# Kernel optimization log

Measured on AMD Instinct MI355X. Metric: run time of the kernel, lower is better.

The kernel has to match this reference:

```python
import jax, jax.numpy as jnp
import numpy as np

D_IN = 768
D_OUT = 768
NUM_HEADS = 12


def setup_inputs() -> dict:
    key = jax.random.key(0)
    kx, kq, kk, kv, ko = jax.random.split(key, 5)
    x = jax.random.normal(kx, (4, 2048, D_IN), dtype=jnp.float32)
    # torch.rand -> uniform [0,1)
    w_query = jax.random.uniform(kq, (D_IN, D_OUT), dtype=jnp.float32)
    w_key = jax.random.uniform(kk, (D_IN, D_OUT), dtype=jnp.float32)
    w_value = jax.random.uniform(kv, (D_IN, D_OUT), dtype=jnp.float32)
    out_proj = jax.random.uniform(ko, (D_IN, D_OUT), dtype=jnp.float32)
    return {"x": x, "w_query": w_query, "w_key": w_key, "w_value": w_value, "out_proj": out_proj}


def reference(x, w_query, w_key, w_value, out_proj):
    b, n, _ = x.shape
    hd = D_OUT // NUM_HEADS  # head_dim
    q = (x @ w_query).reshape(b, n, NUM_HEADS, hd).transpose(0, 2, 1, 3)  # [b,h,n,hd]
    k = (x @ w_key).reshape(b, n, NUM_HEADS, hd).transpose(0, 2, 1, 3)
    v = (x @ w_value).reshape(b, n, NUM_HEADS, hd).transpose(0, 2, 1, 3)
    scores = jnp.einsum('bhqd,bhkd->bhqk', q, k)
    causal = jnp.triu(jnp.ones((n, n), dtype=bool), k=1)
    scores = jnp.where(causal, -jnp.inf, scores)
    attn = jax.nn.softmax(scores / jnp.sqrt(jnp.float32(hd)), axis=-1)
    # dropout p=0.0 -> identity
    ctx = jnp.einsum('bhqk,bhkd->bhqd', attn, v).transpose(0, 2, 1, 3).reshape(b, n, D_OUT)
    return ctx @ out_proj
```

## Files before the change

kernel.cpp:

```cpp
#include <hip/hip_runtime.h>

typedef __bf16 bf16x8 __attribute__((ext_vector_type(8)));
typedef __bf16 bf16x4 __attribute__((ext_vector_type(4)));
typedef float  f32x4  __attribute__((ext_vector_type(4)));

#define MFMA16(a,b,c) __builtin_amdgcn_mfma_f32_16x16x32_bf16((a),(b),(c),0,0,0)

#define AS1(p) (const __attribute__((address_space(1))) void*)(p)
#define AS3(p) (__attribute__((address_space(3))) void*)(p)
#define GLL16(g, l) __builtin_amdgcn_global_load_lds(AS1(g), AS3(l), 16, 0, 0)

__device__ __forceinline__ float fexp2(float x) {
  float r; asm("v_exp_f32 %0, %1" : "=v"(r) : "v"(x)); return r;
}

#define QSCALE 0.18033688011112042f

__global__ __launch_bounds__(256) void k_conv_x(const float* __restrict__ x,
                                                __bf16* __restrict__ xh,
                                                __bf16* __restrict__ xl) {
  int i = blockIdx.x * 256 + threadIdx.x;
  const float4* p = (const float4*)x + (size_t)i * 2;
  float4 a = p[0], b = p[1];
  float v[8] = {a.x, a.y, a.z, a.w, b.x, b.y, b.z, b.w};
  bf16x8 h, l;
#pragma unroll
  for (int j = 0; j < 8; ++j) {
    __bf16 hh = (__bf16)v[j];
    h[j] = hh;
    l[j] = (__bf16)(v[j] - (float)hh);
  }
  *(bf16x8*)(xh + (size_t)i * 8) = h;
  *(bf16x8*)(xl + (size_t)i * 8) = l;
}

__global__ __launch_bounds__(256) void k_conv_w(const float* __restrict__ wq,
                                                const float* __restrict__ wk,
                                                const float* __restrict__ wv,
                                                const float* __restrict__ op,
                                                __bf16* __restrict__ wt_h,
                                                __bf16* __restrict__ wt_l,
                                                __bf16* __restrict__ wot) {
  __shared__ float tile[32][33];
  int bid = blockIdx.x;
  int m = bid / 576, rem = bid % 576;
  int tr = rem / 24, tc = rem % 24;
  const float* src = (m == 0) ? wq : (m == 1) ? wk : (m == 2) ? wv : op;
  int tx = threadIdx.x & 31, ty = threadIdx.x >> 5;
  int r0 = tr * 32, c0 = tc * 32;
#pragma unroll
  for (int j = 0; j < 4; ++j)
    tile[ty + j * 8][tx] = src[(size_t)(r0 + ty + j * 8) * 768 + c0 + tx];
  __syncthreads();
#pragma unroll
  for (int j = 0; j < 4; ++j) {
    float v = tile[tx][ty + j * 8];
    size_t o = (size_t)(c0 + ty + j * 8) * 768 + r0 + tx;
    if (m < 3) {
      size_t oo = (size_t)m * (768 * 768) + o;
      __bf16 h = (__bf16)v;
      wt_h[oo] = h;
      wt_l[oo] = (__bf16)(v - (float)h);
    } else {
      wot[o] = (__bf16)v;
    }
  }
}

__global__ __launch_bounds__(256) void k_qkv_gemm(
    const __bf16* __restrict__ Ah, const __bf16* __restrict__ Al,
    const __bf16* __restrict__ Bh, const __bf16* __restrict__ Bl,
    __bf16* __restrict__ qh_o, __bf16* __restrict__ ql_o,
    __bf16* __restrict__ kh_o, __bf16* __restrict__ kl_o,
    __bf16* __restrict__ vT_o) {
  __shared__ __align__(16) __bf16 AsH[128 * 32];
  __shared__ __align__(16) __bf16 AsL[128 * 32];
  __shared__ __align__(16) __bf16 BsH[128 * 32];
  __shared__ __align__(16) __bf16 BsL[128 * 32];
  int t = threadIdx.x, lane = t & 63, wid = t >> 6;
  int l15 = lane & 15, lh = lane >> 4;
  int bid = blockIdx.x;
  int mt = bid & 63, nt = bid >> 6;
  int m0 = mt * 128, n0 = nt * 128;
  int wr = wid >> 1, wc = wid & 1;
  bool split = (n0 < 1536);
  f32x4 acc[4][4];
#pragma unroll
  for (int i = 0; i < 4; ++i)
#pragma unroll
    for (int j = 0; j < 4; ++j) acc[i][j] = (f32x4){0.f, 0.f, 0.f, 0.f};

  int row0 = t >> 2,        kk0 = (t & 3) * 8;
  int row1 = 64 + (t >> 2), kk1 = kk0;
  char* lA0 = (char*)AsH + wid * 1024; char* lA1 = (char*)AsH + wid * 1024 + 4096;
  char* lAl0 = (char*)AsL + wid * 1024; char* lAl1 = (char*)AsL + wid * 1024 + 4096;
  char* lB0 = (char*)BsH + wid * 1024; char* lB1 = (char*)BsH + wid * 1024 + 4096;
  char* lBl0 = (char*)BsL + wid * 1024; char* lBl1 = (char*)BsL + wid * 1024 + 4096;

  for (int k0 = 0; k0 < 768; k0 += 32) {
    __syncthreads();
    size_t a0 = (size_t)(m0 + row0) * 768 + k0 + kk0;
    size_t a1 = (size_t)(m0 + row1) * 768 + k0 + kk1;
    size_t b0 = (size_t)(n0 + row0) * 768 + k0 + kk0;
    size_t b1 = (size_t)(n0 + row1) * 768 + k0 + kk1;
    GLL16(Ah + a0, lA0);  GLL16(Ah + a1, lA1);
    GLL16(Al + a0, lAl0); GLL16(Al + a1, lAl1);
    GLL16(Bh + b0, lB0);  GLL16(Bh + b1, lB1);
    GLL16(Bl + b0, lBl0); GLL16(Bl + b1, lBl1);
    asm volatile("s_waitcnt vmcnt(0)" ::: "memory");
    __syncthreads();

    bf16x8 af[4], alf[4], bf_[4], blf[4];
#pragma unroll
    for (int i = 0; i < 4; ++i) {
      int aoff = (wr * 64 + i * 16 + l15) * 32 + lh * 8;
      af[i]  = *(const bf16x8*)(AsH + aoff);
      alf[i] = *(const bf16x8*)(AsL + aoff);
      int boff = (wc * 64 + i * 16 + l15) * 32 + lh * 8;
      bf_[i] = *(const bf16x8*)(BsH + boff);
      blf[i] = *(const bf16x8*)(BsL + boff);
    }
#pragma unroll
    for (int i = 0; i < 4; ++i)
#pragma unroll
      for (int j = 0; j < 4; ++j) {
        acc[i][j] = MFMA16(af[i], bf_[j], acc[i][j]);
        if (split) {
          acc[i][j] = MFMA16(af[i], blf[j], acc[i][j]);
          acc[i][j] = MFMA16(alf[i], bf_[j], acc[i][j]);
        }
      }
  }
#pragma unroll
  for (int j = 0; j < 4; ++j) {
    int c = n0 + wc * 64 + j * 16 + l15;
    int which = c / 768; int cc = c - which * 768;
    int hh = cc >> 6, d = cc & 63;
#pragma unroll
    for (int i = 0; i < 4; ++i)
#pragma unroll
      for (int r = 0; r < 4; ++r) {
        int m = m0 + wr * 64 + i * 16 + lh * 4 + r;
        int bb = m >> 11, n = m & 2047;
        float v = acc[i][j][r];
        if (which == 2) {
          vT_o[((size_t)(bb * 12 + hh) * 64 + d) * 2048 + n] = (__bf16)v;
        } else {
          size_t o = ((size_t)(bb * 12 + hh) * 2048 + n) * 64 + d;
          if (which == 0) {
            float vs = v * QSCALE;
            __bf16 hi = (__bf16)vs;
            qh_o[o] = hi; ql_o[o] = (__bf16)(vs - (float)hi);
          } else {
            __bf16 hi = (__bf16)v;
            kh_o[o] = hi; kl_o[o] = (__bf16)(v - (float)hi);
          }
        }
      }
  }
}

__global__ __launch_bounds__(256) void k_attn(
    const __bf16* __restrict__ Qh, const __bf16* __restrict__ Ql,
    const __bf16* __restrict__ Kh, const __bf16* __restrict__ Kl,
    const __bf16* __restrict__ Vt, __bf16* __restrict__ ctx) {
  __shared__ __align__(16) __bf16 Ksh[64 * 64];
  __shared__ __align__(16) __bf16 Ksl[64 * 64];
  __shared__ __align__(16) __bf16 Vs[64 * 64];
  __shared__ __align__(16) __bf16 Pt[4][32 * 64];
  int t = threadIdx.x, lane = t & 63, wid = t >> 6;
  int l15 = lane & 15, lh = lane >> 4;
  int bid = blockIdx.x;
  int bh = bid % 48;
  int qt = 15 - bid / 48;
  int qbase = qt * 128 + wid * 32;
  size_t base = (size_t)bh * (2048 * 64);
  char* ptw = (char*)Pt[wid];

  int skey = t >> 3, sdb = t & 7;
  int ssw = (sdb ^ (skey & 7)) * 8;
  const __bf16* ksrc_h = Kh + base + (size_t)skey * 64 + ssw;
  const __bf16* ksrc_l = Kl + base + (size_t)skey * 64 + ssw;
  const __bf16* vsrc = Vt + base + (size_t)skey * 2048 + ssw;
  char* dKh0 = (char*)Ksh + wid * 1024; char* dKh1 = dKh0 + 4096;
  char* dKl0 = (char*)Ksl + wid * 1024; char* dKl1 = dKl0 + 4096;
  char* dV0  = (char*)Vs  + wid * 1024; char* dV1  = dV0 + 4096;

  bf16x8 qfh[2][2], qfl[2][2];
#pragma unroll
  for (int i = 0; i < 2; ++i)
#pragma unroll
    for (int kk = 0; kk < 2; ++kk) {
      size_t o = (size_t)(qbase + i * 16 + l15) * 64 + kk * 32 + lh * 8;
      qfh[i][kk] = *(const bf16x8*)(Qh + base + o);
      qfl[i][kk] = *(const bf16x8*)(Ql + base + o);
    }

  f32x4 o[2][4];
#pragma unroll
  for (int i = 0; i < 2; ++i)
#pragma unroll
    for (int d = 0; d < 4; ++d) o[i][d] = (f32x4){0.f, 0.f, 0.f, 0.f};
  float mrun[2] = {-1e30f, -1e30f}, lrun[2] = {0.f, 0.f};

  int nIter = 2 * qt + 2;
  for (int it = 0; it < nIter; ++it) {
    int k0 = it * 64;
    __syncthreads();
    GLL16(ksrc_h + (size_t)k0 * 64, dKh0);
    GLL16(ksrc_h + (size_t)k0 * 64 + 2048, dKh1);
    GLL16(ksrc_l + (size_t)k0 * 64, dKl0);
    GLL16(ksrc_l + (size_t)k0 * 64 + 2048, dKl1);
    GLL16(vsrc + k0, dV0);
    GLL16(vsrc + k0 + 32 * 2048, dV1);
    asm volatile("s_waitcnt vmcnt(0)" ::: "memory");
    __syncthreads();

    if (k0 > qbase + 31) continue;

    f32x4 s[4][2];
#pragma unroll
    for (int j = 0; j < 4; ++j)
#pragma unroll
      for (int i = 0; i < 2; ++i) s[j][i] = (f32x4){0.f, 0.f, 0.f, 0.f};
#pragma unroll
    for (int j = 0; j < 4; ++j) {
      int kr = j * 16 + l15;
#pragma unroll
      for (int kk = 0; kk < 2; ++kk) {
        int sw = ((kk * 4 + lh) ^ (kr & 7)) << 4;
        bf16x8 kfh = *(const bf16x8*)((char*)Ksh + kr * 128 + sw);
        bf16x8 kfl = *(const bf16x8*)((char*)Ksl + kr * 128 + sw);
        s[j][0] = MFMA16(kfh, qfh[0][kk], s[j][0]);
        s[j][0] = MFMA16(kfl, qfh[0][kk], s[j][0]);
        s[j][0] = MFMA16(kfh, qfl[0][kk], s[j][0]);
        s[j][1] = MFMA16(kfh, qfh[1][kk], s[j][1]);
        s[j][1] = MFMA16(kfl, qfh[1][kk], s[j][1]);
        s[j][1] = MFMA16(kfh, qfl[1][kk], s[j][1]);
      }
    }

    if (k0 + 63 > qbase) {
#pragma unroll
      for (int j = 0; j < 4; ++j)
#pragma unroll
        for (int i = 0; i < 2; ++i)
#pragma unroll
          for (int r = 0; r < 4; ++r) {
            int key = k0 + j * 16 + lh * 4 + r;
            int qg = qbase + i * 16 + l15;
            if (key > qg) s[j][i][r] = -1e30f;
          }
    }

#pragma unroll
    for (int i = 0; i < 2; ++i) {
      float m01 = fmaxf(fmaxf(s[0][i][0], s[0][i][1]), fmaxf(s[0][i][2], s[0][i][3]));
      float m23 = fmaxf(fmaxf(s[1][i][0], s[1][i][1]), fmaxf(s[1][i][2], s[1][i][3]));
      float m45 = fmaxf(fmaxf(s[2][i][0], s[2][i][1]), fmaxf(s[2][i][2], s[2][i][3]));
      float m67 = fmaxf(fmaxf(s[3][i][0], s[3][i][1]), fmaxf(s[3][i][2], s[3][i][3]));
      float mx = fmaxf(fmaxf(m01, m23), fmaxf(m45, m67));
      mx = fmaxf(mx, __shfl_xor(mx, 16));
      mx = fmaxf(mx, __shfl_xor(mx, 32));
      float mn = fmaxf(mrun[i], mx);
      float alpha = fexp2(mrun[i] - mn);
      mrun[i] = mn;
      float rsum = 0.f;
#pragma unroll
      for (int j = 0; j < 4; ++j)
#pragma unroll
        for (int r = 0; r < 4; ++r) {
          float e = fexp2(s[j][i][r] - mn);
          s[j][i][r] = e;
          rsum += e;
        }
      rsum += __shfl_xor(rsum, 16);
      rsum += __shfl_xor(rsum, 32);
      lrun[i] = lrun[i] * alpha + rsum;
#pragma unroll
      for (int d = 0; d < 4; ++d) o[i][d] *= alpha;
#pragma unroll
      for (int j = 0; j < 4; ++j) {
        bf16x4 pk = { (__bf16)s[j][i][0], (__bf16)s[j][i][1],
                      (__bf16)s[j][i][2], (__bf16)s[j][i][3] };
        int row = 16 * i + l15;
        int boff = (row * 128 + j * 32 + lh * 8) ^ ((l15 & 7) << 4);
        *(bf16x4*)(ptw + boff) = pk;
      }
    }
    asm volatile("" ::: "memory");
    bf16x8 pa[2][2];
#pragma unroll
    for (int i = 0; i < 2; ++i)
#pragma unroll
      for (int kk = 0; kk < 2; ++kk) {
        int row = 16 * i + l15;
        int boff = (row * 128 + kk * 64 + lh * 16) ^ ((l15 & 7) << 4);
        pa[i][kk] = *(const bf16x8*)(ptw + boff);
      }
    asm volatile("" ::: "memory");

#pragma unroll
    for (int dt = 0; dt < 4; ++dt) {
      int dr = dt * 16 + l15;
#pragma unroll
      for (int kk = 0; kk < 2; ++kk) {
        int sw = ((kk * 4 + lh) ^ (dr & 7)) << 4;
        bf16x8 vf = *(const bf16x8*)((char*)Vs + dr * 128 + sw);
        o[0][dt] = MFMA16(vf, pa[0][kk], o[0][dt]);
        o[1][dt] = MFMA16(vf, pa[1][kk], o[1][dt]);
      }
    }
  }

  int b = bh / 12, hh = bh - (bh / 12) * 12;
  float inv[2] = {1.f / lrun[0], 1.f / lrun[1]};
#pragma unroll
  for (int i = 0; i < 2; ++i)
#pragma unroll
    for (int dt = 0; dt < 4; ++dt) {
      bf16x4 cw = { (__bf16)(o[i][dt][0] * inv[i]), (__bf16)(o[i][dt][1] * inv[i]),
                    (__bf16)(o[i][dt][2] * inv[i]), (__bf16)(o[i][dt][3] * inv[i]) };
      int row = 16 * i + l15;
      int boff = (row * 128 + dt * 32 + lh * 8) ^ ((l15 & 7) << 4);
      *(bf16x4*)(ptw + boff) = cw;
    }
  asm volatile("" ::: "memory");
  int lr = lane >> 1, hc = lane & 1;
#pragma unroll
  for (int q16 = 0; q16 < 4; ++q16) {
    int boff = (lr * 128 + hc * 64 + q16 * 16) ^ ((lr & 7) << 4);
    bf16x8 vv = *(const bf16x8*)(ptw + boff);
    *(bf16x8*)(ctx + ((size_t)b * 2048 + qbase + lr) * 768 + hh * 64 + hc * 32 + q16 * 8) = vv;
  }
}

__global__ __launch_bounds__(256) void k_out_gemm(const __bf16* __restrict__ A,
                                                  const __bf16* __restrict__ Bt,
                                                  float* __restrict__ C) {
  __shared__ __align__(16) __bf16 As[128 * 32];
  __shared__ __align__(16) __bf16 Bs[128 * 32];
  int t = threadIdx.x, lane = t & 63, wid = t >> 6;
  int l15 = lane & 15, lh = lane >> 4;
  int bid = blockIdx.x;
  int mt = bid & 63, nt = bid >> 6;
  int m0 = mt * 128, n0 = nt * 128;
  int wr = wid >> 1, wc = wid & 1;
  f32x4 acc[4][4];
#pragma unroll
  for (int i = 0; i < 4; ++i)
#pragma unroll
    for (int j = 0; j < 4; ++j) acc[i][j] = (f32x4){0.f, 0.f, 0.f, 0.f};
  int row0 = t >> 2,        kk0 = (t & 3) * 8;
  int row1 = 64 + (t >> 2), kk1 = kk0;
  char* lA0 = (char*)As + wid * 1024; char* lA1 = (char*)As + wid * 1024 + 4096;
  char* lB0 = (char*)Bs + wid * 1024; char* lB1 = (char*)Bs + wid * 1024 + 4096;

  for (int k0 = 0; k0 < 768; k0 += 32) {
    __syncthreads();
    GLL16(A  + (size_t)(m0 + row0) * 768 + k0 + kk0, lA0);
    GLL16(A  + (size_t)(m0 + row1) * 768 + k0 + kk1, lA1);
    GLL16(Bt + (size_t)(n0 + row0) * 768 + k0 + kk0, lB0);
    GLL16(Bt + (size_t)(n0 + row1) * 768 + k0 + kk1, lB1);
    asm volatile("s_waitcnt vmcnt(0)" ::: "memory");
    __syncthreads();
    bf16x8 af[4], bf_[4];
#pragma unroll
    for (int i = 0; i < 4; ++i) {
      af[i]  = *(const bf16x8*)(As + (wr * 64 + i * 16 + l15) * 32 + lh * 8);
      bf_[i] = *(const bf16x8*)(Bs + (wc * 64 + i * 16 + l15) * 32 + lh * 8);
    }
#pragma unroll
    for (int i = 0; i < 4; ++i)
#pragma unroll
      for (int j = 0; j < 4; ++j) acc[i][j] = MFMA16(af[i], bf_[j], acc[i][j]);
  }
#pragma unroll
  for (int j = 0; j < 4; ++j) {
    int c = n0 + wc * 64 + j * 16 + l15;
#pragma unroll
    for (int i = 0; i < 4; ++i)
#pragma unroll
      for (int r = 0; r < 4; ++r) {
        int m = m0 + wr * 64 + i * 16 + lh * 4 + r;
        C[(size_t)m * 768 + c] = acc[i][j][r];
      }
  }
}

extern "C" void kernel_launch(void* const* d_in, const int* in_sizes, int n_in,
                              void* d_out, int out_size, void* d_ws, size_t ws_size,
                              hipStream_t stream) {
  const float* x  = (const float*)d_in[0];
  const float* wq = (const float*)d_in[1];
  const float* wk = (const float*)d_in[2];
  const float* wv = (const float*)d_in[3];
  const float* op = (const float*)d_in[4];
  float* out = (float*)d_out;

  char* ws = (char*)d_ws;
  const size_t SZ = (size_t)8192 * 768 * 2;
  __bf16* xh   = (__bf16*)ws; ws += SZ;
  __bf16* xl   = (__bf16*)ws; ws += SZ;
  __bf16* wt_h = (__bf16*)ws; ws += (size_t)2304 * 768 * 2;
  __bf16* wt_l = (__bf16*)ws; ws += (size_t)2304 * 768 * 2;
  __bf16* wot  = (__bf16*)ws; ws += (size_t)768 * 768 * 2;
  __bf16* qh   = (__bf16*)ws; ws += SZ;
  __bf16* ql   = (__bf16*)ws; ws += SZ;
  __bf16* kh   = (__bf16*)ws; ws += SZ;
  __bf16* kl   = (__bf16*)ws; ws += SZ;
  __bf16* vT   = (__bf16*)ws; ws += SZ;
  __bf16* ctx  = (__bf16*)ws; ws += SZ;

  hipLaunchKernelGGL(k_conv_x, dim3(3072), dim3(256), 0, stream, x, xh, xl);
  hipLaunchKernelGGL(k_conv_w, dim3(2304), dim3(256), 0, stream,
                     wq, wk, wv, op, wt_h, wt_l, wot);
  hipLaunchKernelGGL(k_qkv_gemm, dim3(64 * 18), dim3(256), 0, stream,
                     xh, xl, wt_h, wt_l, qh, ql, kh, kl, vT);
  hipLaunchKernelGGL(k_attn, dim3(48 * 16), dim3(256), 0, stream,
                     qh, ql, kh, kl, vT, ctx);
  hipLaunchKernelGGL(k_out_gemm, dim3(64 * 6), dim3(256), 0, stream, ctx, wot, out);
}
```

Measured before the change: 288.2 us.

## Double-buffer GEMM and attention loads, swizzle LDS, use fp16 Q/K scores

The QKV, output and attention kernels move to double-buffered LDS staging, so the next K-tile's global-to-LDS loads are issued before computing on the current one. The GEMM shared tiles get an XOR swizzle to reduce bank conflicts. Low-half loads are skipped for unsplit V/out tiles. Q and K are now stored as single fp16 values instead of bf16 hi/lo pairs, cutting the QK^T MFMAs from three to one and halving K traffic, at the cost of lower precision and possible fp16 overflow if Q·K values grow large. Doubling LDS per block may lower occupancy.

```diff
diff --git a/kernel.cpp b/kernel.cpp
--- a/kernel.cpp
+++ b/kernel.cpp
@@ -1,10 +1,12 @@
 #include <hip/hip_runtime.h>
 
-typedef __bf16 bf16x8 __attribute__((ext_vector_type(8)));
-typedef __bf16 bf16x4 __attribute__((ext_vector_type(4)));
-typedef float  f32x4  __attribute__((ext_vector_type(4)));
-
-#define MFMA16(a,b,c) __builtin_amdgcn_mfma_f32_16x16x32_bf16((a),(b),(c),0,0,0)
+typedef __bf16    bf16x8 __attribute__((ext_vector_type(8)));
+typedef __bf16    bf16x4 __attribute__((ext_vector_type(4)));
+typedef _Float16  f16x8  __attribute__((ext_vector_type(8)));
+typedef float     f32x4  __attribute__((ext_vector_type(4)));
+
+#define MFMA16(a,b,c)  __builtin_amdgcn_mfma_f32_16x16x32_bf16((a),(b),(c),0,0,0)
+#define MFMAF16(a,b,c) __builtin_amdgcn_mfma_f32_16x16x32_f16((a),(b),(c),0,0,0)
 
 #define AS1(p) (const __attribute__((address_space(1))) void*)(p)
 #define AS3(p) (__attribute__((address_space(3))) void*)(p)
@@ -70,13 +72,12 @@
 __global__ __launch_bounds__(256) void k_qkv_gemm(
     const __bf16* __restrict__ Ah, const __bf16* __restrict__ Al,
     const __bf16* __restrict__ Bh, const __bf16* __restrict__ Bl,
-    __bf16* __restrict__ qh_o, __bf16* __restrict__ ql_o,
-    __bf16* __restrict__ kh_o, __bf16* __restrict__ kl_o,
+    _Float16* __restrict__ qf_o, _Float16* __restrict__ kf_o,
     __bf16* __restrict__ vT_o) {
-  __shared__ __align__(16) __bf16 AsH[128 * 32];
-  __shared__ __align__(16) __bf16 AsL[128 * 32];
-  __shared__ __align__(16) __bf16 BsH[128 * 32];
-  __shared__ __align__(16) __bf16 BsL[128 * 32];
+  __shared__ __align__(16) __bf16 AsH[2][128 * 32];
+  __shared__ __align__(16) __bf16 AsL[2][128 * 32];
+  __shared__ __align__(16) __bf16 BsH[2][128 * 32];
+  __shared__ __align__(16) __bf16 BsL[2][128 * 32];
   int t = threadIdx.x, lane = t & 63, wid = t >> 6;
   int l15 = lane & 15, lh = lane >> 4;
   int bid = blockIdx.x;
@@ -90,35 +91,47 @@
 #pragma unroll
     for (int j = 0; j < 4; ++j) acc[i][j] = (f32x4){0.f, 0.f, 0.f, 0.f};
 
-  int row0 = t >> 2,        kk0 = (t & 3) * 8;
-  int row1 = 64 + (t >> 2), kk1 = kk0;
-  char* lA0 = (char*)AsH + wid * 1024; char* lA1 = (char*)AsH + wid * 1024 + 4096;
-  char* lAl0 = (char*)AsL + wid * 1024; char* lAl1 = (char*)AsL + wid * 1024 + 4096;
-  char* lB0 = (char*)BsH + wid * 1024; char* lB1 = (char*)BsH + wid * 1024 + 4096;
-  char* lBl0 = (char*)BsL + wid * 1024; char* lBl1 = (char*)BsL + wid * 1024 + 4096;
-
-  for (int k0 = 0; k0 < 768; k0 += 32) {
-    __syncthreads();
-    size_t a0 = (size_t)(m0 + row0) * 768 + k0 + kk0;
-    size_t a1 = (size_t)(m0 + row1) * 768 + k0 + kk1;
-    size_t b0 = (size_t)(n0 + row0) * 768 + k0 + kk0;
-    size_t b1 = (size_t)(n0 + row1) * 768 + k0 + kk1;
-    GLL16(Ah + a0, lA0);  GLL16(Ah + a1, lA1);
-    GLL16(Al + a0, lAl0); GLL16(Al + a1, lAl1);
-    GLL16(Bh + b0, lB0);  GLL16(Bh + b1, lB1);
-    GLL16(Bl + b0, lBl0); GLL16(Bl + b1, lBl1);
-    asm volatile("s_waitcnt vmcnt(0)" ::: "memory");
-    __syncthreads();
+  int row0 = t >> 2;
+  int kkA = (((t & 3) ^ ((row0 >> 1) & 3)) << 3);
+  char* lAH[2] = {(char*)AsH[0] + wid * 1024, (char*)AsH[1] + wid * 1024};
+  char* lAL[2] = {(char*)AsL[0] + wid * 1024, (char*)AsL[1] + wid * 1024};
+  char* lBH[2] = {(char*)BsH[0] + wid * 1024, (char*)BsH[1] + wid * 1024};
+  char* lBL[2] = {(char*)BsL[0] + wid * 1024, (char*)BsL[1] + wid * 1024};
+
+#define QKV_STAGE(bb, k0s) do {                                              \
+    size_t a0 = (size_t)(m0 + row0) * 768 + (k0s) + kkA;                     \
+    size_t a1 = a0 + (size_t)64 * 768;                                       \
+    size_t b0 = (size_t)(n0 + row0) * 768 + (k0s) + kkA;                     \
+    size_t b1 = b0 + (size_t)64 * 768;                                       \
+    GLL16(Ah + a0, lAH[bb]); GLL16(Ah + a1, lAH[bb] + 4096);                 \
+    GLL16(Bh + b0, lBH[bb]); GLL16(Bh + b1, lBH[bb] + 4096);                 \
+    if (split) {                                                             \
+      GLL16(Al + a0, lAL[bb]); GLL16(Al + a1, lAL[bb] + 4096);               \
+      GLL16(Bl + b0, lBL[bb]); GLL16(Bl + b1, lBL[bb] + 4096);               \
+    }                                                                        \
+  } while (0)
+
+  QKV_STAGE(0, 0);
+  asm volatile("s_waitcnt vmcnt(0)" ::: "memory");
+  __syncthreads();
+
+  for (int tt = 0; tt < 24; ++tt) {
+    int cur = tt & 1;
+    if (tt < 23) QKV_STAGE(cur ^ 1, (tt + 1) * 32);
 
     bf16x8 af[4], alf[4], bf_[4], blf[4];
 #pragma unroll
     for (int i = 0; i < 4; ++i) {
-      int aoff = (wr * 64 + i * 16 + l15) * 32 + lh * 8;
-      af[i]  = *(const bf16x8*)(AsH + aoff);
-      alf[i] = *(const bf16x8*)(AsL + aoff);
-      int boff = (wc * 64 + i * 16 + l15) * 32 + lh * 8;
-      bf_[i] = *(const bf16x8*)(BsH + boff);
-      blf[i] = *(const bf16x8*)(BsL + boff);
+      int rowA = wr * 64 + i * 16 + l15;
+      int aoff = rowA * 64 + (((lh ^ (rowA >> 1)) & 3) << 4);
+      int rowB = wc * 64 + i * 16 + l15;
+      int boff = rowB * 64 + (((lh ^ (rowB >> 1)) & 3) << 4);
+      af[i]  = *(const bf16x8*)((char*)AsH[cur] + aoff);
+      bf_[i] = *(const bf16x8*)((char*)BsH[cur] + boff);
+      if (split) {
+        alf[i] = *(const bf16x8*)((char*)AsL[cur] + aoff);
+        blf[i] = *(const bf16x8*)((char*)BsL[cur] + boff);
+      }
     }
 #pragma unroll
     for (int i = 0; i < 4; ++i)
@@ -130,7 +143,11 @@
           acc[i][j] = MFMA16(alf[i], bf_[j], acc[i][j]);
         }
       }
-  }
+    asm volatile("s_waitcnt vmcnt(0)" ::: "memory");
+    __syncthreads();
+  }
+#undef QKV_STAGE
+
 #pragma unroll
   for (int j = 0; j < 4; ++j) {
     int c = n0 + wc * 64 + j * 16 + l15;
@@ -147,26 +164,18 @@
           vT_o[((size_t)(bb * 12 + hh) * 64 + d) * 2048 + n] = (__bf16)v;
         } else {
           size_t o = ((size_t)(bb * 12 + hh) * 2048 + n) * 64 + d;
-          if (which == 0) {
-            float vs = v * QSCALE;
-            __bf16 hi = (__bf16)vs;
-            qh_o[o] = hi; ql_o[o] = (__bf16)(vs - (float)hi);
-          } else {
-            __bf16 hi = (__bf16)v;
-            kh_o[o] = hi; kl_o[o] = (__bf16)(v - (float)hi);
-          }
+          if (which == 0) qf_o[o] = (_Float16)(v * QSCALE);
+          else            kf_o[o] = (_Float16)v;
         }
       }
   }
 }
 
 __global__ __launch_bounds__(256) void k_attn(
-    const __bf16* __restrict__ Qh, const __bf16* __restrict__ Ql,
-    const __bf16* __restrict__ Kh, const __bf16* __restrict__ Kl,
+    const _Float16* __restrict__ Qf, const _Float16* __restrict__ Kf,
     const __bf16* __restrict__ Vt, __bf16* __restrict__ ctx) {
-  __shared__ __align__(16) __bf16 Ksh[64 * 64];
-  __shared__ __align__(16) __bf16 Ksl[64 * 64];
-  __shared__ __align__(16) __bf16 Vs[64 * 64];
+  __shared__ __align__(16) _Float16 Ks[2][64 * 64];
+  __shared__ __align__(16) __bf16 Vs[2][64 * 64];
   __shared__ __align__(16) __bf16 Pt[4][32 * 64];
   int t = threadIdx.x, lane = t & 63, wid = t >> 6;
   int l15 = lane & 15, lh = lane >> 4;
@@ -179,22 +188,25 @@
 
   int skey = t >> 3, sdb = t & 7;
   int ssw = (sdb ^ (skey & 7)) * 8;
-  const __bf16* ksrc_h = Kh + base + (size_t)skey * 64 + ssw;
-  const __bf16* ksrc_l = Kl + base + (size_t)skey * 64 + ssw;
+  const _Float16* ksrc = Kf + base + (size_t)skey * 64 + ssw;
   const __bf16* vsrc = Vt + base + (size_t)skey * 2048 + ssw;
-  char* dKh0 = (char*)Ksh + wid * 1024; char* dKh1 = dKh0 + 4096;
-  char* dKl0 = (char*)Ksl + wid * 1024; char* dKl1 = dKl0 + 4096;
-  char* dV0  = (char*)Vs  + wid * 1024; char* dV1  = dV0 + 4096;
-
-  bf16x8 qfh[2][2], qfl[2][2];
+  char* dK[2] = {(char*)Ks[0] + wid * 1024, (char*)Ks[1] + wid * 1024};
+  char* dV[2] = {(char*)Vs[0] + wid * 1024, (char*)Vs[1] + wid * 1024};
+
+#define ATT_STAGE(bb, k0s) do {                                    \
+    GLL16(ksrc + (size_t)(k0s) * 64, dK[bb]);                      \
+    GLL16(ksrc + (size_t)(k0s) * 64 + 2048, dK[bb] + 4096);        \
+    GLL16(vsrc + (k0s), dV[bb]);                                   \
+    GLL16(vsrc + (k0s) + 32 * 2048, dV[bb] + 4096);                \
+  } while (0)
+
+  f16x8 qf[2][2];
 #pragma unroll
   for (int i = 0; i < 2; ++i)
 #pragma unroll
-    for (int kk = 0; kk < 2; ++kk) {
-      size_t o = (size_t)(qbase + i * 16 + l15) * 64 + kk * 32 + lh * 8;
-      qfh[i][kk] = *(const bf16x8*)(Qh + base + o);
-      qfl[i][kk] = *(const bf16x8*)(Ql + base + o);
-    }
+    for (int kk = 0; kk < 2; ++kk)
+      qf[i][kk] = *(const f16x8*)(Qf + base +
+          (size_t)(qbase + i * 16 + l15) * 64 + kk * 32 + lh * 8);
 
   f32x4 o[2][4];
 #pragma unroll
@@ -204,114 +216,109 @@
   float mrun[2] = {-1e30f, -1e30f}, lrun[2] = {0.f, 0.f};
 
   int nIter = 2 * qt + 2;
+  ATT_STAGE(0, 0);
+  asm volatile("s_waitcnt vmcnt(0)" ::: "memory");
+  __syncthreads();
+
   for (int it = 0; it < nIter; ++it) {
+    int cur = it & 1;
     int k0 = it * 64;
-    __syncthreads();
-    GLL16(ksrc_h + (size_t)k0 * 64, dKh0);
-    GLL16(ksrc_h + (size_t)k0 * 64 + 2048, dKh1);
-    GLL16(ksrc_l + (size_t)k0 * 64, dKl0);
-    GLL16(ksrc_l + (size_t)k0 * 64 + 2048, dKl1);
-    GLL16(vsrc + k0, dV0);
-    GLL16(vsrc + k0 + 32 * 2048, dV1);
+    if (it + 1 < nIter) ATT_STAGE(cur ^ 1, k0 + 64);
+
+    if (k0 <= qbase + 31) {
+      f32x4 s[4][2];
+#pragma unroll
+      for (int j = 0; j < 4; ++j)
+#pragma unroll
+        for (int i = 0; i < 2; ++i) s[j][i] = (f32x4){0.f, 0.f, 0.f, 0.f};
+#pragma unroll
+      for (int j = 0; j < 4; ++j) {
+        int kr = j * 16 + l15;
+#pragma unroll
+        for (int kk = 0; kk < 2; ++kk) {
+          int sw = ((kk * 4 + lh) ^ (kr & 7)) << 4;
+          f16x8 kf = *(const f16x8*)((char*)Ks[cur] + kr * 128 + sw);
+          s[j][0] = MFMAF16(kf, qf[0][kk], s[j][0]);
+          s[j][1] = MFMAF16(kf, qf[1][kk], s[j][1]);
+        }
+      }
+
+      if (k0 + 63 > qbase) {
+#pragma unroll
+        for (int j = 0; j < 4; ++j)
+#pragma unroll
+          for (int i = 0; i < 2; ++i)
+#pragma unroll
+            for (int r = 0; r < 4; ++r) {
+              int key = k0 + j * 16 + lh * 4 + r;
+              int qg = qbase + i * 16 + l15;
+              if (key > qg) s[j][i][r] = -1e30f;
+            }
+      }
+
+#pragma unroll
+      for (int i = 0; i < 2; ++i) {
+        float m01 = fmaxf(fmaxf(s[0][i][0], s[0][i][1]), fmaxf(s[0][i][2], s[0][i][3]));
+        float m23 = fmaxf(fmaxf(s[1][i][0], s[1][i][1]), fmaxf(s[1][i][2], s[1][i][3]));
+        float m45 = fmaxf(fmaxf(s[2][i][0], s[2][i][1]), fmaxf(s[2][i][2], s[2][i][3]));
+        float m67 = fmaxf(fmaxf(s[3][i][0], s[3][i][1]), fmaxf(s[3][i][2], s[3][i][3]));
+        float mx = fmaxf(fmaxf(m01, m23), fmaxf(m45, m67));
+        mx = fmaxf(mx, __shfl_xor(mx, 16));
+        mx = fmaxf(mx, __shfl_xor(mx, 32));
+        float mn = fmaxf(mrun[i], mx);
+        float alpha = fexp2(mrun[i] - mn);
+        mrun[i] = mn;
+        float rsum = 0.f;
+#pragma unroll
+        for (int j = 0; j < 4; ++j)
+#pragma unroll
+          for (int r = 0; r < 4; ++r) {
+            float e = fexp2(s[j][i][r] - mn);
+            s[j][i][r] = e;
+            rsum += e;
+          }
+        rsum += __shfl_xor(rsum, 16);
+        rsum += __shfl_xor(rsum, 32);
+        lrun[i] = lrun[i] * alpha + rsum;
+#pragma unroll
+        for (int d = 0; d < 4; ++d) o[i][d] *= alpha;
+#pragma unroll
+        for (int j = 0; j < 4; ++j) {
+          bf16x4 pk = { (__bf16)s[j][i][0], (__bf16)s[j][i][1],
+                        (__bf16)s[j][i][2], (__bf16)s[j][i][3] };
+          int row = 16 * i + l15;
+          int boff = (row * 128 + j * 32 + lh * 8) ^ ((l15 & 7) << 4);
+          *(bf16x4*)(ptw + boff) = pk;
+        }
+      }
+      asm volatile("" ::: "memory");
+      bf16x8 pa[2][2];
+#pragma unroll
+      for (int i = 0; i < 2; ++i)
+#pragma unroll
+        for (int kk = 0; kk < 2; ++kk) {
+          int row = 16 * i + l15;
+          int boff = (row * 128 + kk * 64 + lh * 16) ^ ((l15 & 7) << 4);
+          pa[i][kk] = *(const bf16x8*)(ptw + boff);
+        }
+      asm volatile("" ::: "memory");
+
+#pragma unroll
+      for (int dt = 0; dt < 4; ++dt) {
+        int dr = dt * 16 + l15;
+#pragma unroll
+        for (int kk = 0; kk < 2; ++kk) {
+          int sw = ((kk * 4 + lh) ^ (dr & 7)) << 4;
+          bf16x8 vf = *(const bf16x8*)((char*)Vs[cur] + dr * 128 + sw);
+          o[0][dt] = MFMA16(vf, pa[0][kk], o[0][dt]);
+          o[1][dt] = MFMA16(vf, pa[1][kk], o[1][dt]);
+        }
+      }
+    }
     asm volatile("s_waitcnt vmcnt(0)" ::: "memory");
     __syncthreads();
-
-    if (k0 > qbase + 31) continue;
-
-    f32x4 s[4][2];
-#pragma unroll
-    for (int j = 0; j < 4; ++j)
-#pragma unroll
-      for (int i = 0; i < 2; ++i) s[j][i] = (f32x4){0.f, 0.f, 0.f, 0.f};
-#pragma unroll
-    for (int j = 0; j < 4; ++j) {
-      int kr = j * 16 + l15;
-#pragma unroll
-      for (int kk = 0; kk < 2; ++kk) {
-        int sw = ((kk * 4 + lh) ^ (kr & 7)) << 4;
-        bf16x8 kfh = *(const bf16x8*)((char*)Ksh + kr * 128 + sw);
-        bf16x8 kfl = *(const bf16x8*)((char*)Ksl + kr * 128 + sw);
-        s[j][0] = MFMA16(kfh, qfh[0][kk], s[j][0]);
-        s[j][0] = MFMA16(kfl, qfh[0][kk], s[j][0]);
-        s[j][0] = MFMA16(kfh, qfl[0][kk], s[j][0]);
-        s[j][1] = MFMA16(kfh, qfh[1][kk], s[j][1]);
-        s[j][1] = MFMA16(kfl, qfh[1][kk], s[j][1]);
-        s[j][1] = MFMA16(kfh, qfl[1][kk], s[j][1]);
-      }
-    }
-
-    if (k0 + 63 > qbase) {
-#pragma unroll
-      for (int j = 0; j < 4; ++j)
-#pragma unroll
-        for (int i = 0; i < 2; ++i)
-#pragma unroll
-          for (int r = 0; r < 4; ++r) {
-            int key = k0 + j * 16 + lh * 4 + r;
-            int qg = qbase + i * 16 + l15;
-            if (key > qg) s[j][i][r] = -1e30f;
-          }
-    }
-
-#pragma unroll
-    for (int i = 0; i < 2; ++i) {
-      float m01 = fmaxf(fmaxf(s[0][i][0], s[0][i][1]), fmaxf(s[0][i][2], s[0][i][3]));
-      float m23 = fmaxf(fmaxf(s[1][i][0], s[1][i][1]), fmaxf(s[1][i][2], s[1][i][3]));
-      float m45 = fmaxf(fmaxf(s[2][i][0], s[2][i][1]), fmaxf(s[2][i][2], s[2][i][3]));
-      float m67 = fmaxf(fmaxf(s[3][i][0], s[3][i][1]), fmaxf(s[3][i][2], s[3][i][3]));
-      float mx = fmaxf(fmaxf(m01, m23), fmaxf(m45, m67));
-      mx = fmaxf(mx, __shfl_xor(mx, 16));
-      mx = fmaxf(mx, __shfl_xor(mx, 32));
-      float mn = fmaxf(mrun[i], mx);
-      float alpha = fexp2(mrun[i] - mn);
-      mrun[i] = mn;
-      float rsum = 0.f;
-#pragma unroll
-      for (int j = 0; j < 4; ++j)
-#pragma unroll
-        for (int r = 0; r < 4; ++r) {
-          float e = fexp2(s[j][i][r] - mn);
-          s[j][i][r] = e;
-          rsum += e;
-        }
-      rsum += __shfl_xor(rsum, 16);
-      rsum += __shfl_xor(rsum, 32);
-      lrun[i] = lrun[i] * alpha + rsum;
-#pragma unroll
-      for (int d = 0; d < 4; ++d) o[i][d] *= alpha;
-#pragma unroll
-      for (int j = 0; j < 4; ++j) {
-        bf16x4 pk = { (__bf16)s[j][i][0], (__bf16)s[j][i][1],
-                      (__bf16)s[j][i][2], (__bf16)s[j][i][3] };
-        int row = 16 * i + l15;
-        int boff = (row * 128 + j * 32 + lh * 8) ^ ((l15 & 7) << 4);
-        *(bf16x4*)(ptw + boff) = pk;
-      }
-    }
-    asm volatile("" ::: "memory");
-    bf16x8 pa[2][2];
-#pragma unroll
-    for (int i = 0; i < 2; ++i)
-#pragma unroll
-      for (int kk = 0; kk < 2; ++kk) {
-        int row = 16 * i + l15;
-        int boff = (row * 128 + kk * 64 + lh * 16) ^ ((l15 & 7) << 4);
-        pa[i][kk] = *(const bf16x8*)(ptw + boff);
-      }
-    asm volatile("" ::: "memory");
-
-#pragma unroll
-    for (int dt = 0; dt < 4; ++dt) {
-      int dr = dt * 16 + l15;
-#pragma unroll
-      for (int kk = 0; kk < 2; ++kk) {
-        int sw = ((kk * 4 + lh) ^ (dr & 7)) << 4;
-        bf16x8 vf = *(const bf16x8*)((char*)Vs + dr * 128 + sw);
-        o[0][dt] = MFMA16(vf, pa[0][kk], o[0][dt]);
-        o[1][dt] = MFMA16(vf, pa[1][kk], o[1][dt]);
-      }
-    }
-  }
+  }
+#undef ATT_STAGE
 
   int b = bh / 12, hh = bh - (bh / 12) * 12;
   float inv[2] = {1.f / lrun[0], 1.f / lrun[1]};
@@ -338,8 +345,8 @@
 __global__ __launch_bounds__(256) void k_out_gemm(const __bf16* __restrict__ A,
                                                   const __bf16* __restrict__ Bt,
                                                   float* __restrict__ C) {
-  __shared__ __align__(16) __bf16 As[128 * 32];
-  __shared__ __align__(16) __bf16 Bs[128 * 32];
+  __shared__ __align__(16) __bf16 As[2][128 * 32];
+  __shared__ __align__(16) __bf16 Bs[2][128 * 32];
   int t = threadIdx.x, lane = t & 63, wid = t >> 6;
   int l15 = lane & 15, lh = lane >> 4;
   int bid = blockIdx.x;
@@ -351,30 +358,44 @@
   for (int i = 0; i < 4; ++i)
 #pragma unroll
     for (int j = 0; j < 4; ++j) acc[i][j] = (f32x4){0.f, 0.f, 0.f, 0.f};
-  int row0 = t >> 2,        kk0 = (t & 3) * 8;
-  int row1 = 64 + (t >> 2), kk1 = kk0;
-  char* lA0 = (char*)As + wid * 1024; char* lA1 = (char*)As + wid * 1024 + 4096;
-  char* lB0 = (char*)Bs + wid * 1024; char* lB1 = (char*)Bs + wid * 1024 + 4096;
-
-  for (int k0 = 0; k0 < 768; k0 += 32) {
-    __syncthreads();
-    GLL16(A  + (size_t)(m0 + row0) * 768 + k0 + kk0, lA0);
-    GLL16(A  + (size_t)(m0 + row1) * 768 + k0 + kk1, lA1);
-    GLL16(Bt + (size_t)(n0 + row0) * 768 + k0 + kk0, lB0);
-    GLL16(Bt + (size_t)(n0 + row1) * 768 + k0 + kk1, lB1);
+  int row0 = t >> 2;
+  int kkA = (((t & 3) ^ ((row0 >> 1) & 3)) << 3);
+  char* lA[2] = {(char*)As[0] + wid * 1024, (char*)As[1] + wid * 1024};
+  char* lB[2] = {(char*)Bs[0] + wid * 1024, (char*)Bs[1] + wid * 1024};
+
+#define OUT_STAGE(bb, k0s) do {                                              \
+    size_t a0 = (size_t)(m0 + row0) * 768 + (k0s) + kkA;                     \
+    size_t b0 = (size_t)(n0 + row0) * 768 + (k0s) + kkA;                     \
+    GLL16(A + a0, lA[bb]);  GLL16(A + a0 + (size_t)64 * 768, lA[bb] + 4096); \
+    GLL16(Bt + b0, lB[bb]); GLL16(Bt + b0 + (size_t)64 * 768, lB[bb] + 4096);\
+  } while (0)
+
+  OUT_STAGE(0, 0);
+  asm volatile("s_waitcnt vmcnt(0)" ::: "memory");
+  __syncthreads();
+
+  for (int tt = 0; tt < 24; ++tt) {
+    int cur = tt & 1;
+    if (tt < 23) OUT_STAGE(cur ^ 1, (tt + 1) * 32);
+    bf16x8 af[4], bf_[4];
+#pragma unroll
+    for (int i = 0; i < 4; ++i) {
+      int rowA = wr * 64 + i * 16 + l15;
+      int aoff = rowA * 64 + (((lh ^ (rowA >> 1)) & 3) << 4);
+      int rowB = wc * 64 + i * 16 + l15;
+      int boff = rowB * 64 + (((lh ^ (rowB >> 1)) & 3) << 4);
+      af[i]  = *(const bf16x8*)((char*)As[cur] + aoff);
+      bf_[i] = *(const bf16x8*)((char*)Bs[cur] + boff);
+    }
+#pragma unroll
+    for (int i = 0; i < 4; ++i)
+#pragma unroll
+      for (int j = 0; j < 4; ++j) acc[i][j] = MFMA16(af[i], bf_[j], acc[i][j]);
     asm volatile("s_waitcnt vmcnt(0)" ::: "memory");
     __syncthreads();
-    bf16x8 af[4], bf_[4];
-#pragma unroll
-    for (int i = 0; i < 4; ++i) {
-      af[i]  = *(const bf16x8*)(As + (wr * 64 + i * 16 + l15) * 32 + lh * 8);
-      bf_[i] = *(const bf16x8*)(Bs + (wc * 64 + i * 16 + l15) * 32 + lh * 8);
-    }
-#pragma unroll
-    for (int i = 0; i < 4; ++i)
-#pragma unroll
-      for (int j = 0; j < 4; ++j) acc[i][j] = MFMA16(af[i], bf_[j], acc[i][j]);
-  }
+  }
+#undef OUT_STAGE
+
 #pragma unroll
   for (int j = 0; j < 4; ++j) {
     int c = n0 + wc * 64 + j * 16 + l15;
@@ -400,24 +421,22 @@
 
   char* ws = (char*)d_ws;
   const size_t SZ = (size_t)8192 * 768 * 2;
-  __bf16* xh   = (__bf16*)ws; ws += SZ;
-  __bf16* xl   = (__bf16*)ws; ws += SZ;
-  __bf16* wt_h = (__bf16*)ws; ws += (size_t)2304 * 768 * 2;
-  __bf16* wt_l = (__bf16*)ws; ws += (size_t)2304 * 768 * 2;
-  __bf16* wot  = (__bf16*)ws; ws += (size_t)768 * 768 * 2;
-  __bf16* qh   = (__bf16*)ws; ws += SZ;
-  __bf16* ql   = (__bf16*)ws; ws += SZ;
-  __bf16* kh   = (__bf16*)ws; ws += SZ;
-  __bf16* kl   = (__bf16*)ws; ws += SZ;
-  __bf16* vT   = (__bf16*)ws; ws += SZ;
-  __bf16* ctx  = (__bf16*)ws; ws += SZ;
+  __bf16* xh     = (__bf16*)ws;    ws += SZ;
+  __bf16* xl     = (__bf16*)ws;    ws += SZ;
+  __bf16* wt_h   = (__bf16*)ws;    ws += (size_t)2304 * 768 * 2;
+  __bf16* wt_l   = (__bf16*)ws;    ws += (size_t)2304 * 768 * 2;
+  __bf16* wot    = (__bf16*)ws;    ws += (size_t)768 * 768 * 2;
+  _Float16* qf   = (_Float16*)ws;  ws += SZ;
+  _Float16* kf   = (_Float16*)ws;  ws += SZ;
+  __bf16* vT     = (__bf16*)ws;    ws += SZ;
+  __bf16* ctx    = (__bf16*)ws;    ws += SZ;
 
   hipLaunchKernelGGL(k_conv_x, dim3(3072), dim3(256), 0, stream, x, xh, xl);
   hipLaunchKernelGGL(k_conv_w, dim3(2304), dim3(256), 0, stream,
                      wq, wk, wv, op, wt_h, wt_l, wot);
   hipLaunchKernelGGL(k_qkv_gemm, dim3(64 * 18), dim3(256), 0, stream,
-                     xh, xl, wt_h, wt_l, qh, ql, kh, kl, vT);
+                     xh, xl, wt_h, wt_l, qf, kf, vT);
   hipLaunchKernelGGL(k_attn, dim3(48 * 16), dim3(256), 0, stream,
-                     qh, ql, kh, kl, vT, ctx);
+                     qf, kf, vT, ctx);
   hipLaunchKernelGGL(k_out_gemm, dim3(64 * 6), dim3(256), 0, stream, ctx, wot, out);
 }
```

Measured after the change: 259.9 us. -9.8%, faster.
